# Kernel optimization log

Hardware: AMD Instinct MI355X
Metric: run time of the kernel (lower is better)

The kernel has to match this reference:

```python
import jax, jax.numpy as jnp
import numpy as np

N_NODES = 100000
N_EDGES = 1600000
D_IN = 128
D_OUT = 128


def setup_inputs() -> dict:
    key = jax.random.key(0)
    k1, k2, k3, k4, k5 = jax.random.split(key, 5)
    x = jax.random.normal(k1, (N_NODES, D_IN), dtype=jnp.float32)
    weight = jax.random.normal(k2, (D_IN, D_OUT), dtype=jnp.float32)
    edge_src = jax.random.randint(k3, (N_EDGES,), 0, N_NODES, dtype=jnp.int32)
    edge_dst = jax.random.randint(k4, (N_EDGES,), 0, N_NODES, dtype=jnp.int32)
    edge_val = jax.random.uniform(k5, (N_EDGES,), dtype=jnp.float32)
    return {"x": x, "weight": weight, "edge_src": edge_src,
            "edge_dst": edge_dst, "edge_val": edge_val}


def reference(x, weight, edge_src, edge_dst, edge_val):
    # SpMM: T[dst] += val * x[src]   (adjacency @ features)
    msgs = x[edge_src] * edge_val[:, None]              # [E, D_IN]
    T = jax.ops.segment_sum(msgs, edge_dst, num_segments=N_NODES)  # [N, D_IN]
    # Dense projection: Z = T @ W
    Z = T @ weight                                      # [N, D_OUT]
    return Z
```

## Files before the change

### kernel.cpp

```cpp
#include <hip/hip_runtime.h>

#define N_NODES 100000
#define N_EDGES 1600000
#define D 128
#define CAP 48

typedef __attribute__((ext_vector_type(8))) short bf16x8;
typedef __attribute__((ext_vector_type(4))) float f32x4;
typedef __attribute__((ext_vector_type(2))) float f32x2;
typedef unsigned short ushort_t;

__device__ __forceinline__ ushort_t bf(float f) {
    unsigned u = __float_as_uint(f);
    return (ushort_t)((u + 0x7fffu + ((u >> 16) & 1u)) >> 16);
}

#define ZERO_BLOCKS 391
__global__ __launch_bounds__(256) void setup_kernel(int* __restrict__ cnt,
                                                    const float* __restrict__ W,
                                                    ushort_t* __restrict__ Wt) {
    int b = blockIdx.x;
    if (b < ZERO_BLOCKS) {
        int i = b * 256 + threadIdx.x;
        if (i < N_NODES) cnt[i] = 0;
    } else {
        int i = (b - ZERO_BLOCKS) * 256 + threadIdx.x;
        int n = i >> 7, k = i & 127;
        Wt[i] = bf(W[k * D + n]);
    }
}

#define GEMM_BLOCKS 1563
#define SCAT_BLOCKS 6250
#define LP (D + 8)
__global__ __launch_bounds__(256) void gemm_scatter_kernel(
        const float* __restrict__ X, const ushort_t* __restrict__ Wt,
        ushort_t* __restrict__ Y,
        const int* __restrict__ src, const int* __restrict__ dst,
        const float* __restrict__ val,
        int* __restrict__ cnt, unsigned* __restrict__ epack) {
    __shared__ ushort_t lx[64][LP];
    __shared__ ushort_t lw[D][LP];
    const int bb = blockIdx.x;
    const int tid = threadIdx.x;

    if (bb % 5 == 0) {
        const int gb = bb / 5;
        const long long row0 = (long long)gb * 64;

#pragma unroll
        for (int it = 0; it < 8; ++it) {
            int c = tid + it * 256;
            int r = c >> 4, c16 = c & 15;
            *(ulonglong2*)&lw[r][c16 * 8] = *(const ulonglong2*)(Wt + r * D + c16 * 8);
        }
#pragma unroll
        for (int it = 0; it < 8; ++it) {
            int c = tid + it * 256;
            int r = c >> 5, c4 = c & 31;
            long long gr = row0 + r;
            if (gr >= N_NODES) gr = 0;
            float4 v = *(const float4*)(X + gr * D + c4 * 4);
            ushort4 b4 = make_ushort4(bf(v.x), bf(v.y), bf(v.z), bf(v.w));
            *(ushort4*)&lx[r][c4 * 4] = b4;
        }
        __syncthreads();

        const int wave = tid >> 6, lane = tid & 63;
        const int mrow = lane & 15, quad = lane >> 4;

        f32x4 acc[8];
#pragma unroll
        for (int nt = 0; nt < 8; ++nt) acc[nt] = (f32x4){0.f, 0.f, 0.f, 0.f};

#pragma unroll
        for (int kc = 0; kc < 4; ++kc) {
            bf16x8 a = *(const bf16x8*)&lx[wave * 16 + mrow][kc * 32 + quad * 8];
#pragma unroll
            for (int nt = 0; nt < 8; ++nt) {
                bf16x8 b = *(const bf16x8*)&lw[nt * 16 + mrow][kc * 32 + quad * 8];
                acc[nt] = __builtin_amdgcn_mfma_f32_16x16x32_bf16(a, b, acc[nt], 0, 0, 0);
            }
        }

        const long long baserow = row0 + wave * 16 + quad * 4;
#pragma unroll
        for (int nt = 0; nt < 8; ++nt)
#pragma unroll
            for (int r = 0; r < 4; ++r) {
                long long grow = baserow + r;
                if (grow < N_NODES)
                    Y[grow * D + nt * 16 + mrow] = bf(acc[nt][r]);
            }
    } else {
        int sb = bb - bb / 5 - 1;
        int e = sb * 256 + tid;
        if (e < N_EDGES) {
            int d = dst[e];
            int slot = atomicAdd(&cnt[d], 1);
            if (slot < CAP) {
                unsigned q = (unsigned)(val[e] * 32767.0f + 0.5f);
                epack[d * CAP + slot] = ((unsigned)src[e]) | (q << 17);
            }
        }
    }
}

__global__ __launch_bounds__(256) void gather_kernel(
        const unsigned* __restrict__ Yu, const int* __restrict__ cnt,
        const unsigned* __restrict__ epack, float* __restrict__ Z) {
    const int n = blockIdx.x * 4 + (threadIdx.x >> 6);
    const int lane = threadIdx.x & 63;

    int c = cnt[n];
    c = (c < CAP) ? c : CAP;
    const int e0 = n * CAP, e1 = e0 + c;
    float ax = 0.f, ay = 0.f;
    const float q2f = 1.0f / 32767.0f;

    for (int e = e0; e < e1; e += 16) {
        unsigned p[16];
#pragma unroll
        for (int j = 0; j < 16; ++j) {
            int idx = e + j;
            idx = (idx < e1) ? idx : (e1 - 1);
            p[j] = __builtin_nontemporal_load(epack + idx);
        }
        unsigned y[16];
#pragma unroll
        for (int j = 0; j < 16; ++j)
            y[j] = Yu[((p[j] & 0x1ffffu) << 6) + lane];
#pragma unroll
        for (int j = 0; j < 16; ++j) {
            float v = (e + j < e1) ? (float)(p[j] >> 17) * q2f : 0.f;
            ax += v * __uint_as_float(y[j] << 16);
            ay += v * __uint_as_float(y[j] & 0xffff0000u);
        }
    }

    f32x2 r; r[0] = ax; r[1] = ay;
    __builtin_nontemporal_store(r, (f32x2*)Z + (long long)n * 64 + lane);
}

extern "C" void kernel_launch(void* const* d_in, const int* in_sizes, int n_in,
                              void* d_out, int out_size, void* d_ws, size_t ws_size,
                              hipStream_t stream) {
    const float* x    = (const float*)d_in[0];
    const float* W    = (const float*)d_in[1];
    const int*   esrc = (const int*)  d_in[2];
    const int*   edst = (const int*)  d_in[3];
    const float* eval_= (const float*)d_in[4];
    float*       Z    = (float*)d_out;

    char* w = (char*)d_ws;
    int*      cnt   = (int*)     (w + 0);
    unsigned* epack = (unsigned*)(w + 400000);
    ushort_t* Wt    = (ushort_t*)(w + 19600000);
    ushort_t* Yu    = (ushort_t*)(w + 19632768);

    setup_kernel<<<ZERO_BLOCKS + 64, 256, 0, stream>>>(cnt, W, Wt);
    gemm_scatter_kernel<<<GEMM_BLOCKS + SCAT_BLOCKS, 256, 0, stream>>>(
        x, Wt, Yu, esrc, edst, eval_, cnt, epack);
    gather_kernel<<<N_NODES / 4, 256, 0, stream>>>((const unsigned*)Yu, cnt, epack, Z);
}
```

Baseline: 243.6 us.

## Split fused GEMM/scatter kernel and process four edges per scatter thread

Replaces the interleaved GEMM+scatter launch with two separate kernels: a scatter kernel where each thread handles four edges with loads batched ahead of the atomics, and a standalone GEMM kernel. This removes the per-block branch on block role and the large shared-memory footprint that the scatter blocks had to reserve, and it gives each scatter thread more memory-level parallelism. The cost is an extra kernel launch and the loss of overlap between the GEMM and the scatter phases.

```diff
diff --git a/kernel.cpp b/kernel.cpp
--- a/kernel.cpp
+++ b/kernel.cpp
@@ -30,80 +30,98 @@
     }
 }
 
-#define GEMM_BLOCKS 1563
-#define SCAT_BLOCKS 6250
-#define LP (D + 8)
-__global__ __launch_bounds__(256) void gemm_scatter_kernel(
-        const float* __restrict__ X, const ushort_t* __restrict__ Wt,
-        ushort_t* __restrict__ Y,
+#define SCAT_BLOCKS 1563
+__global__ __launch_bounds__(256) void scatter_kernel(
         const int* __restrict__ src, const int* __restrict__ dst,
         const float* __restrict__ val,
         int* __restrict__ cnt, unsigned* __restrict__ epack) {
-    __shared__ ushort_t lx[64][LP];
-    __shared__ ushort_t lw[D][LP];
-    const int bb = blockIdx.x;
-    const int tid = threadIdx.x;
+    const int base = blockIdx.x * 1024 + threadIdx.x;
 
-    if (bb % 5 == 0) {
-        const int gb = bb / 5;
-        const long long row0 = (long long)gb * 64;
-
+    if (blockIdx.x < SCAT_BLOCKS - 1) {
+        int d0 = dst[base];          int d1 = dst[base + 256];
+        int d2 = dst[base + 512];    int d3 = dst[base + 768];
+        int s0 = src[base];          int s1 = src[base + 256];
+        int s2 = src[base + 512];    int s3 = src[base + 768];
+        float v0 = val[base];        float v1 = val[base + 256];
+        float v2 = val[base + 512];  float v3 = val[base + 768];
+        int t0 = atomicAdd(&cnt[d0], 1);
+        int t1 = atomicAdd(&cnt[d1], 1);
+        int t2 = atomicAdd(&cnt[d2], 1);
+        int t3 = atomicAdd(&cnt[d3], 1);
+        if (t0 < CAP) epack[d0 * CAP + t0] = ((unsigned)s0) | (((unsigned)(v0 * 32767.0f + 0.5f)) << 17);
+        if (t1 < CAP) epack[d1 * CAP + t1] = ((unsigned)s1) | (((unsigned)(v1 * 32767.0f + 0.5f)) << 17);
+        if (t2 < CAP) epack[d2 * CAP + t2] = ((unsigned)s2) | (((unsigned)(v2 * 32767.0f + 0.5f)) << 17);
+        if (t3 < CAP) epack[d3 * CAP + t3] = ((unsigned)s3) | (((unsigned)(v3 * 32767.0f + 0.5f)) << 17);
+    } else {
 #pragma unroll
-        for (int it = 0; it < 8; ++it) {
-            int c = tid + it * 256;
-            int r = c >> 4, c16 = c & 15;
-            *(ulonglong2*)&lw[r][c16 * 8] = *(const ulonglong2*)(Wt + r * D + c16 * 8);
-        }
-#pragma unroll
-        for (int it = 0; it < 8; ++it) {
-            int c = tid + it * 256;
-            int r = c >> 5, c4 = c & 31;
-            long long gr = row0 + r;
-            if (gr >= N_NODES) gr = 0;
-            float4 v = *(const float4*)(X + gr * D + c4 * 4);
-            ushort4 b4 = make_ushort4(bf(v.x), bf(v.y), bf(v.z), bf(v.w));
-            *(ushort4*)&lx[r][c4 * 4] = b4;
-        }
-        __syncthreads();
-
-        const int wave = tid >> 6, lane = tid & 63;
-        const int mrow = lane & 15, quad = lane >> 4;
-
-        f32x4 acc[8];
-#pragma unroll
-        for (int nt = 0; nt < 8; ++nt) acc[nt] = (f32x4){0.f, 0.f, 0.f, 0.f};
-
-#pragma unroll
-        for (int kc = 0; kc < 4; ++kc) {
-            bf16x8 a = *(const bf16x8*)&lx[wave * 16 + mrow][kc * 32 + quad * 8];
-#pragma unroll
-            for (int nt = 0; nt < 8; ++nt) {
-                bf16x8 b = *(const bf16x8*)&lw[nt * 16 + mrow][kc * 32 + quad * 8];
-                acc[nt] = __builtin_amdgcn_mfma_f32_16x16x32_bf16(a, b, acc[nt], 0, 0, 0);
-            }
-        }
-
-        const long long baserow = row0 + wave * 16 + quad * 4;
-#pragma unroll
-        for (int nt = 0; nt < 8; ++nt)
-#pragma unroll
-            for (int r = 0; r < 4; ++r) {
-                long long grow = baserow + r;
-                if (grow < N_NODES)
-                    Y[grow * D + nt * 16 + mrow] = bf(acc[nt][r]);
-            }
-    } else {
-        int sb = bb - bb / 5 - 1;
-        int e = sb * 256 + tid;
-        if (e < N_EDGES) {
-            int d = dst[e];
-            int slot = atomicAdd(&cnt[d], 1);
-            if (slot < CAP) {
-                unsigned q = (unsigned)(val[e] * 32767.0f + 0.5f);
-                epack[d * CAP + slot] = ((unsigned)src[e]) | (q << 17);
+        for (int j = 0; j < 4; ++j) {
+            int e = base + j * 256;
+            if (e < N_EDGES) {
+                int d = dst[e];
+                int slot = atomicAdd(&cnt[d], 1);
+                if (slot < CAP) {
+                    unsigned q = (unsigned)(val[e] * 32767.0f + 0.5f);
+                    epack[d * CAP + slot] = ((unsigned)src[e]) | (q << 17);
+                }
             }
         }
     }
+}
+
+#define GEMM_BLOCKS 1563
+#define LP (D + 8)
+__global__ __launch_bounds__(256) void gemm_kernel(
+        const float* __restrict__ X, const ushort_t* __restrict__ Wt,
+        ushort_t* __restrict__ Y) {
+    __shared__ ushort_t lx[64][LP];
+    __shared__ ushort_t lw[D][LP];
+    const int tid = threadIdx.x;
+    const long long row0 = (long long)blockIdx.x * 64;
+
+#pragma unroll
+    for (int it = 0; it < 8; ++it) {
+        int c = tid + it * 256;
+        int r = c >> 4, c16 = c & 15;
+        *(ulonglong2*)&lw[r][c16 * 8] = *(const ulonglong2*)(Wt + r * D + c16 * 8);
+    }
+#pragma unroll
+    for (int it = 0; it < 8; ++it) {
+        int c = tid + it * 256;
+        int r = c >> 5, c4 = c & 31;
+        long long gr = row0 + r;
+        if (gr >= N_NODES) gr = 0;
+        float4 v = *(const float4*)(X + gr * D + c4 * 4);
+        ushort4 b4 = make_ushort4(bf(v.x), bf(v.y), bf(v.z), bf(v.w));
+        *(ushort4*)&lx[r][c4 * 4] = b4;
+    }
+    __syncthreads();
+
+    const int wave = tid >> 6, lane = tid & 63;
+    const int mrow = lane & 15, quad = lane >> 4;
+
+    f32x4 acc[8];
+#pragma unroll
+    for (int nt = 0; nt < 8; ++nt) acc[nt] = (f32x4){0.f, 0.f, 0.f, 0.f};
+
+#pragma unroll
+    for (int kc = 0; kc < 4; ++kc) {
+        bf16x8 a = *(const bf16x8*)&lx[wave * 16 + mrow][kc * 32 + quad * 8];
+#pragma unroll
+        for (int nt = 0; nt < 8; ++nt) {
+            bf16x8 b = *(const bf16x8*)&lw[nt * 16 + mrow][kc * 32 + quad * 8];
+            acc[nt] = __builtin_amdgcn_mfma_f32_16x16x32_bf16(a, b, acc[nt], 0, 0, 0);
+        }
+    }
+
+    const long long baserow = row0 + wave * 16 + quad * 4;
+#pragma unroll
+    for (int nt = 0; nt < 8; ++nt)
+#pragma unroll
+        for (int r = 0; r < 4; ++r) {
+            long long grow = baserow + r;
+            if (grow < N_NODES)
+                Y[grow * D + nt * 16 + mrow] = bf(acc[nt][r]);
+        }
 }
 
 __global__ __launch_bounds__(256) void gather_kernel(
@@ -159,7 +177,7 @@
     ushort_t* Yu    = (ushort_t*)(w + 19632768);
 
     setup_kernel<<<ZERO_BLOCKS + 64, 256, 0, stream>>>(cnt, W, Wt);
-    gemm_scatter_kernel<<<GEMM_BLOCKS + SCAT_BLOCKS, 256, 0, stream>>>(
-        x, Wt, Yu, esrc, edst, eval_, cnt, epack);
+    scatter_kernel<<<SCAT_BLOCKS, 256, 0, stream>>>(esrc, edst, eval_, cnt, epack);
+    gemm_kernel<<<GEMM_BLOCKS, 256, 0, stream>>>(x, Wt, Yu);
     gather_kernel<<<N_NODES / 4, 256, 0, stream>>>((const unsigned*)Yu, cnt, epack, Z);
 }
```

After: 298.9 us. 22.7% more time.
